# Performance work log

Measured on AMD Instinct MI355X. Metric: run time of the kernel, lower is better.

## Reference

```python
import jax, jax.numpy as jnp
import numpy as np

DIM = 1024

def setup_inputs() -> dict:
    key = jax.random.key(0)
    k1, k2, k3, k4 = jax.random.split(key, 4)
    B, L, D = 32, 2048, DIM
    x = jax.random.normal(k1, (B, D), dtype=jnp.float32)
    context = jax.random.normal(k2, (B, L, D), dtype=jnp.float32)
    # linear_concatWa: Linear(2*dim, dim, bias=False) -> weight [dim, 2*dim]
    Wa = jax.random.normal(k3, (D, 2 * D), dtype=jnp.float32) * (1.0 / np.sqrt(2 * D))
    # linear_concatVa: Linear(dim, 1, bias=False) -> weight [1, dim]
    Va = jax.random.normal(k4, (1, D), dtype=jnp.float32) * (1.0 / np.sqrt(D))
    return {"x": x, "context": context, "Wa": Wa, "Va": Va}


def reference(x, context, Wa, Va):
    # concat-mode additive (Bahdanau) attention.
    # Wa @ cat(ht, hs) == ht @ Wa[:, :D].T + hs @ Wa[:, D:].T  (avoids materializing concat)
    D = x.shape[-1]
    Wa_t, Wa_s = Wa[:, :D], Wa[:, D:]              # each [D, D]
    ht_proj = jnp.einsum('bd,kd->bk', x, Wa_t)     # [B, D]
    hs_proj = jnp.einsum('bld,kd->blk', context, Wa_s)  # [B, L, D]
    hidden = jnp.tanh(ht_proj[:, None, :] + hs_proj)    # [B, L, D]
    scores = jnp.einsum('blk,ok->bl', hidden, Va)       # [B, L]  (Va: [1, D])
    attn = jax.nn.softmax(scores, axis=-1)               # [B, L]
    weighted = jnp.einsum('bl,bld->bd', attn, context)   # [B, D]
    return weighted, attn
```

## Files before the change

### kernel.cpp

```cpp
#include <hip/hip_runtime.h>
#include <hip/hip_bf16.h>
#include <cstdint>
#include <cstddef>

#define DIM 1024
#define B_SZ 32
#define L_SZ 2048

#define BM 128
#define BN 128

#define CVT_BLOCKS 8192
#define HT_BLOCKS  512
#define WA_BLOCKS  512

typedef __attribute__((ext_vector_type(8))) short bf16x8;
typedef __attribute__((ext_vector_type(4))) float floatx4;

static __device__ __forceinline__ unsigned cvt2_bf16_rne(float a, float b) {
    unsigned ua = __builtin_bit_cast(unsigned, a);
    unsigned ub = __builtin_bit_cast(unsigned, b);
    ua = (ua + 0x7FFFu + ((ua >> 16) & 1u)) >> 16;
    ub = (ub + 0x7FFFu + ((ub >> 16) & 1u)) >> 16;
    return ua | (ub << 16);
}

static __device__ __forceinline__ float bf2f(unsigned u16) {
    return __builtin_bit_cast(float, u16 << 16);
}

static __device__ __forceinline__ float tanh_fast(float x) {
    float e = __expf(2.0f * x);
    return 1.0f - 2.0f * __builtin_amdgcn_rcpf(e + 1.0f);
}

static __device__ __forceinline__ void gld_lds16(const void* g, void* lds) {
    __builtin_amdgcn_global_load_lds(
        (const __attribute__((address_space(1))) unsigned int*)g,
        (__attribute__((address_space(3))) unsigned int*)lds,
        16, 0, 0);
}

__global__ __launch_bounds__(256) void pre_kernel(
    const float* __restrict__ x, const float* __restrict__ ctx,
    const float* __restrict__ Wa,
    unsigned short* __restrict__ ctxB, unsigned short* __restrict__ WaB,
    float* __restrict__ ht, float* __restrict__ scores,
    float* __restrict__ weighted)
{
    const int bid = blockIdx.x, t = threadIdx.x;

    if (bid < CVT_BLOCKS) {
        const long n4 = (long)B_SZ * L_SZ * DIM / 4;
        const long stride = (long)CVT_BLOCKS * 256;
        for (long i = (long)bid * 256 + t; i < n4; i += stride) {
            const float4 a = ((const float4*)ctx)[i];
            ((uint2*)ctxB)[i] =
                make_uint2(cvt2_bf16_rne(a.x, a.y), cvt2_bf16_rne(a.z, a.w));
        }
    } else if (bid < CVT_BLOCKS + HT_BLOCKS) {
        const int lb = bid - CVT_BLOCKS;
        const int gi = lb * 256 + t;
        if (gi < B_SZ * L_SZ) scores[gi] = 0.f;
        const int b = lb >> 4, kb = lb & 15;
        __shared__ float xs[DIM];
        for (int i = t; i < DIM; i += 256) xs[i] = x[b * DIM + i];
        __syncthreads();
        const int wave = t >> 6, lane = t & 63;
        const float4* xs4 = (const float4*)xs;
        for (int kk = 0; kk < 16; ++kk) {
            const int k = kb * 64 + wave * 16 + kk;
            const float4* wr = (const float4*)(Wa + (size_t)k * (2 * DIM));
            float s = 0.f;
            #pragma unroll
            for (int d = 0; d < DIM / 4; d += 64) {
                const float4 w4 = wr[d + lane];
                const float4 x4 = xs4[d + lane];
                s += w4.x * x4.x + w4.y * x4.y + w4.z * x4.z + w4.w * x4.w;
            }
            #pragma unroll
            for (int off = 32; off > 0; off >>= 1) s += __shfl_xor(s, off);
            if (lane == 0) ht[b * DIM + k] = s;
        }
    } else {
        const int lb = bid - CVT_BLOCKS - HT_BLOCKS;
        const int i = lb * 256 + t;
        if (i < B_SZ * DIM) weighted[i] = 0.f;
        const int k = i >> 7, dc = i & 127;
        const float* s = Wa + (size_t)k * (2 * DIM) + DIM + dc * 8;
        const float4 a = ((const float4*)s)[0];
        const float4 b4 = ((const float4*)s)[1];
        uint4 o;
        o.x = cvt2_bf16_rne(a.x, a.y);
        o.y = cvt2_bf16_rne(a.z, a.w);
        o.z = cvt2_bf16_rne(b4.x, b4.y);
        o.w = cvt2_bf16_rne(b4.z, b4.w);
        ((uint4*)(WaB + (size_t)k * DIM + dc * 8))[0] = o;
    }
}

__global__ __launch_bounds__(256) void gemm_score_bf16(
    const unsigned short* __restrict__ A, const unsigned short* __restrict__ Bm,
    const float* __restrict__ Va, const float* __restrict__ ht,
    float* __restrict__ scores)
{
    __shared__ __align__(16) unsigned short As[BM * 64];
    __shared__ __align__(16) unsigned short Bs[BN * 64];
    const int t = threadIdx.x;
    const int n0 = blockIdx.x * BN;
    const int m0 = blockIdx.y * BM;
    const int lane = t & 63, wave = t >> 6;
    const int l15 = lane & 15, quad = lane >> 4;
    const int wm = (wave >> 1) * 64, wn = (wave & 1) * 64;

    const int lr = lane >> 3;
    const int lc = (lane & 7) ^ lr;
    const size_t aRow = (size_t)(m0 + wave * 32 + lr);
    const size_t bRow = (size_t)(n0 + wave * 32 + lr);

    floatx4 acc[4][4];
    #pragma unroll
    for (int i = 0; i < 4; ++i)
        #pragma unroll
        for (int j = 0; j < 4; ++j) acc[i][j] = (floatx4)0.f;

    for (int k0 = 0; k0 < DIM; k0 += 64) {
        #pragma unroll
        for (int q = 0; q < 4; ++q) {
            gld_lds16(A + (aRow + q * 8) * DIM + k0 + lc * 8,
                      &As[(wave * 32 + q * 8) * 64]);
            gld_lds16(Bm + (bRow + q * 8) * DIM + k0 + lc * 8,
                      &Bs[(wave * 32 + q * 8) * 64]);
        }
        __syncthreads();

        bf16x8 af[2][4], bv[2][4];
        #pragma unroll
        for (int kb = 0; kb < 2; ++kb) {
            #pragma unroll
            for (int i = 0; i < 4; ++i) {
                const int r = wm + i * 16 + l15;
                const int c = (kb * 4 + quad) ^ (r & 7);
                af[kb][i] = *(const bf16x8*)&As[r * 64 + c * 8];
            }
            #pragma unroll
            for (int j = 0; j < 4; ++j) {
                const int r = wn + j * 16 + l15;
                const int c = (kb * 4 + quad) ^ (r & 7);
                bv[kb][j] = *(const bf16x8*)&Bs[r * 64 + c * 8];
            }
        }
        #pragma unroll
        for (int kb = 0; kb < 2; ++kb)
            #pragma unroll
            for (int i = 0; i < 4; ++i)
                #pragma unroll
                for (int j = 0; j < 4; ++j)
                    acc[i][j] = __builtin_amdgcn_mfma_f32_16x16x32_bf16(
                        af[kb][i], bv[kb][j], acc[i][j], 0, 0, 0);
        __syncthreads();
    }

    const int bb = m0 >> 11;
    float htv[4], vav[4];
    #pragma unroll
    for (int j = 0; j < 4; ++j) {
        const int ng = n0 + wn + j * 16 + l15;
        htv[j] = ht[bb * DIM + ng];
        vav[j] = Va[ng];
    }
    #pragma unroll
    for (int i = 0; i < 4; ++i) {
        #pragma unroll
        for (int r = 0; r < 4; ++r) {
            float s = 0.f;
            #pragma unroll
            for (int j = 0; j < 4; ++j)
                s += tanh_fast(acc[i][j][r] + htv[j]) * vav[j];
            s += __shfl_xor(s, 8);
            s += __shfl_xor(s, 4);
            s += __shfl_xor(s, 2);
            s += __shfl_xor(s, 1);
            if (l15 == 0)
                atomicAdd(&scores[m0 + wm + i * 16 + quad * 4 + r], s);
        }
    }
}

__global__ __launch_bounds__(256) void post_kernel(
    const float* __restrict__ scores, const unsigned short* __restrict__ ctxB,
    float* __restrict__ attn, float* __restrict__ weighted)
{
    const int b = blockIdx.x, slice = blockIdx.y, t = threadIdx.x;
    const float* sc = scores + b * L_SZ;
    __shared__ float red[256];
    __shared__ float att[128];

    float m = -1e30f;
    for (int l = t; l < L_SZ; l += 256) m = fmaxf(m, sc[l]);
    red[t] = m; __syncthreads();
    for (int s = 128; s > 0; s >>= 1) { if (t < s) red[t] = fmaxf(red[t], red[t + s]); __syncthreads(); }
    m = red[0]; __syncthreads();
    float sum = 0.f;
    for (int l = t; l < L_SZ; l += 256) sum += __expf(sc[l] - m);
    red[t] = sum; __syncthreads();
    for (int s = 128; s > 0; s >>= 1) { if (t < s) red[t] += red[t + s]; __syncthreads(); }
    const float inv = 1.0f / red[0];

    const int l0 = slice * 128;
    if (t < 128) {
        const float av = __expf(sc[l0 + t] - m) * inv;
        att[t] = av;
        attn[b * L_SZ + l0 + t] = av;
    }
    __syncthreads();

    const unsigned short* cb = ctxB + ((size_t)b * L_SZ + l0) * DIM + t * 4;
    float a0 = 0.f, a1 = 0.f, a2 = 0.f, a3 = 0.f;
    for (int l = 0; l < 128; ++l) {
        const float a = att[l];
        const uint2 v = *(const uint2*)(cb + (size_t)l * DIM);
        a0 += a * bf2f(v.x & 0xFFFFu);
        a1 += a * bf2f(v.x >> 16);
        a2 += a * bf2f(v.y & 0xFFFFu);
        a3 += a * bf2f(v.y >> 16);
    }
    float* o = weighted + b * DIM + t * 4;
    atomicAdd(o + 0, a0);
    atomicAdd(o + 1, a1);
    atomicAdd(o + 2, a2);
    atomicAdd(o + 3, a3);
}

#define LDS_STRIDE 40
__global__ __launch_bounds__(256) void ht_kernel_fb(const float* __restrict__ x,
                                                    const float* __restrict__ Wa,
                                                    float* __restrict__ ht,
                                                    float* __restrict__ scores) {
    const int b = blockIdx.x, kb = blockIdx.y, t = threadIdx.x;
    const int gidx = (b * 16 + kb) * 256 + t;
    if (gidx < B_SZ * L_SZ) scores[gidx] = 0.f;
    __shared__ float xs[DIM];
    for (int i = t; i < DIM; i += 256) xs[i] = x[b * DIM + i];
    __syncthreads();
    const int wave = t >> 6, lane = t & 63;
    for (int kk = 0; kk < 16; ++kk) {
        const int k = kb * 64 + wave * 16 + kk;
        const float* wr = Wa + (size_t)k * (2 * DIM);
        float s = 0.f;
        #pragma unroll
        for (int d = 0; d < DIM; d += 64) s += xs[d + lane] * wr[d + lane];
        #pragma unroll
        for (int off = 32; off > 0; off >>= 1) s += __shfl_xor(s, off);
        if (lane == 0) ht[b * DIM + k] = s;
    }
}

__global__ __launch_bounds__(256, 2) void gemm_score_kernel(
    const float* __restrict__ ctx, const float* __restrict__ Wa,
    const float* __restrict__ Va, const float* __restrict__ ht,
    float* __restrict__ scores)
{
    __shared__ unsigned short As[BM * LDS_STRIDE];
    __shared__ unsigned short Bs[BN * LDS_STRIDE];
    const int t = threadIdx.x;
    const int n0 = blockIdx.x * BN;
    const int m0 = blockIdx.y * BM;
    const int lane = t & 63, wave = t >> 6;
    const int l15 = lane & 15, quad = lane >> 4;
    const int wm = (wave >> 1) * 64, wn = (wave & 1) * 64;
    const int srow = t >> 3;
    const int scol = (t & 7) * 4;
    const float* aBase = ctx + (size_t)(m0 + srow) * DIM + scol;
    const float* bBase = Wa + (size_t)(n0 + srow) * (2 * DIM) + DIM + scol;

    floatx4 acc[4][4];
    #pragma unroll
    for (int i = 0; i < 4; ++i)
        #pragma unroll
        for (int j = 0; j < 4; ++j) acc[i][j] = (floatx4)0.f;

    for (int k0 = 0; k0 < DIM; k0 += 32) {
        __syncthreads();
        #pragma unroll
        for (int r = 0; r < 4; ++r) {
            const float4 va = *(const float4*)(aBase + (size_t)(r * 32) * DIM + k0);
            const float4 vb = *(const float4*)(bBase + (size_t)(r * 32) * (2 * DIM) + k0);
            *(uint2*)&As[(srow + r * 32) * LDS_STRIDE + scol] =
                make_uint2(cvt2_bf16_rne(va.x, va.y), cvt2_bf16_rne(va.z, va.w));
            *(uint2*)&Bs[(srow + r * 32) * LDS_STRIDE + scol] =
                make_uint2(cvt2_bf16_rne(vb.x, vb.y), cvt2_bf16_rne(vb.z, vb.w));
        }
        __syncthreads();
        bf16x8 af[4], bfr[4];
        #pragma unroll
        for (int i = 0; i < 4; ++i)
            af[i] = *(const bf16x8*)&As[(wm + i * 16 + l15) * LDS_STRIDE + quad * 8];
        #pragma unroll
        for (int j = 0; j < 4; ++j)
            bfr[j] = *(const bf16x8*)&Bs[(wn + j * 16 + l15) * LDS_STRIDE + quad * 8];
        #pragma unroll
        for (int i = 0; i < 4; ++i)
            #pragma unroll
            for (int j = 0; j < 4; ++j)
                acc[i][j] = __builtin_amdgcn_mfma_f32_16x16x32_bf16(af[i], bfr[j], acc[i][j], 0, 0, 0);
    }
    const int bb = m0 >> 11;
    float htv[4], vav[4];
    #pragma unroll
    for (int j = 0; j < 4; ++j) {
        const int ng = n0 + wn + j * 16 + l15;
        htv[j] = ht[bb * DIM + ng];
        vav[j] = Va[ng];
    }
    #pragma unroll
    for (int i = 0; i < 4; ++i) {
        #pragma unroll
        for (int r = 0; r < 4; ++r) {
            float s = 0.f;
            #pragma unroll
            for (int j = 0; j < 4; ++j)
                s += tanh_fast(acc[i][j][r] + htv[j]) * vav[j];
            s += __shfl_xor(s, 8);
            s += __shfl_xor(s, 4);
            s += __shfl_xor(s, 2);
            s += __shfl_xor(s, 1);
            if (l15 == 0)
                atomicAdd(&scores[m0 + wm + i * 16 + quad * 4 + r], s);
        }
    }
}

__global__ __launch_bounds__(256) void post_kernel_fb(
    const float* __restrict__ scores, const float* __restrict__ ctx,
    float* __restrict__ attn, float* __restrict__ weighted)
{
    const int b = blockIdx.x, slice = blockIdx.y, t = threadIdx.x;
    const float* sc = scores + b * L_SZ;
    __shared__ float red[256];
    __shared__ float att[128];
    float m = -1e30f;
    for (int l = t; l < L_SZ; l += 256) m = fmaxf(m, sc[l]);
    red[t] = m; __syncthreads();
    for (int s = 128; s > 0; s >>= 1) { if (t < s) red[t] = fmaxf(red[t], red[t + s]); __syncthreads(); }
    m = red[0]; __syncthreads();
    float sum = 0.f;
    for (int l = t; l < L_SZ; l += 256) sum += __expf(sc[l] - m);
    red[t] = sum; __syncthreads();
    for (int s = 128; s > 0; s >>= 1) { if (t < s) red[t] += red[t + s]; __syncthreads(); }
    const float inv = 1.0f / red[0];
    const int l0 = slice * 128;
    if (t < 128) {
        const float av = __expf(sc[l0 + t] - m) * inv;
        att[t] = av;
        attn[b * L_SZ + l0 + t] = av;
    }
    __syncthreads();
    const float* cb = ctx + ((size_t)b * L_SZ + l0) * DIM + t * 4;
    float4 w = make_float4(0.f, 0.f, 0.f, 0.f);
    for (int l = 0; l < 128; ++l) {
        const float a = att[l];
        const float4 c = *(const float4*)(cb + (size_t)l * DIM);
        w.x += a * c.x; w.y += a * c.y; w.z += a * c.z; w.w += a * c.w;
    }
    float* o = weighted + b * DIM + t * 4;
    atomicAdd(o + 0, w.x);
    atomicAdd(o + 1, w.y);
    atomicAdd(o + 2, w.z);
    atomicAdd(o + 3, w.w);
}

__global__ __launch_bounds__(256) void zero_weighted_fb(float* __restrict__ weighted) {
    const int i = blockIdx.x * 256 + threadIdx.x;
    if (i < B_SZ * DIM) weighted[i] = 0.f;
}

extern "C" void kernel_launch(void* const* d_in, const int* in_sizes, int n_in,
                              void* d_out, int out_size, void* d_ws, size_t ws_size,
                              hipStream_t stream) {
    const float* x   = (const float*)d_in[0];
    const float* ctx = (const float*)d_in[1];
    const float* Wa  = (const float*)d_in[2];
    const float* Va  = (const float*)d_in[3];

    float* out      = (float*)d_out;
    float* weighted = out;
    float* attn     = out + B_SZ * DIM;

    float* scores = (float*)d_ws;
    float* ht     = scores + B_SZ * L_SZ;

    const size_t base = (size_t)(B_SZ * L_SZ + B_SZ * DIM) * sizeof(float);
    const size_t need = base + (size_t)DIM * DIM * 2
                      + (size_t)B_SZ * L_SZ * DIM * 2;

    if (ws_size >= need) {
        unsigned short* WaB  = (unsigned short*)((char*)d_ws + base);
        unsigned short* ctxB = WaB + (size_t)DIM * DIM;
        pre_kernel<<<CVT_BLOCKS + HT_BLOCKS + WA_BLOCKS, 256, 0, stream>>>(
            x, ctx, Wa, ctxB, WaB, ht, scores, weighted);
        gemm_score_bf16<<<dim3(DIM / BN, (B_SZ * L_SZ) / BM), 256, 0, stream>>>(
            ctxB, WaB, Va, ht, scores);
        post_kernel<<<dim3(B_SZ, 16), 256, 0, stream>>>(scores, ctxB, attn, weighted);
    } else {
        ht_kernel_fb<<<dim3(B_SZ, 16), 256, 0, stream>>>(x, Wa, ht, scores);
        zero_weighted_fb<<<(B_SZ * DIM + 255) / 256, 256, 0, stream>>>(weighted);
        gemm_score_kernel<<<dim3(DIM / BN, (B_SZ * L_SZ) / BM), 256, 0, stream>>>(
            ctx, Wa, Va, ht, scores);
        post_kernel_fb<<<dim3(B_SZ, 16), 256, 0, stream>>>(scores, ctx, attn, weighted);
    }
}
```

Measured before the change: 603.3 us.

## Fuse context bf16 conversion into GEMM A-tile load, drop bf16 copy

Removes the separate pass that converts the whole fp32 context tensor to a bf16 workspace copy. The GEMM now loads fp32 context, rounds it to bf16 in registers and writes it into the swizzled LDS tile, and the post kernel reads fp32 context directly. This is meant to cut the large write-then-reread of a bf16 context copy. In exchange, the GEMM fetches twice as many bytes per A tile, repeated across column blocks, and uses register staging instead of direct-to-LDS loads. Rounding changes from round-to-nearest-even to round-half-up.

```diff
diff --git a/kernel.cpp b/kernel.cpp
--- a/kernel.cpp
+++ b/kernel.cpp
@@ -10,7 +10,6 @@
 #define BM 128
 #define BN 128
 
-#define CVT_BLOCKS 8192
 #define HT_BLOCKS  512
 #define WA_BLOCKS  512
 
@@ -25,8 +24,10 @@
     return ua | (ub << 16);
 }
 
-static __device__ __forceinline__ float bf2f(unsigned u16) {
-    return __builtin_bit_cast(float, u16 << 16);
+static __device__ __forceinline__ unsigned pk2_bf16_rhu(float a, float b) {
+    const unsigned ua = __builtin_bit_cast(unsigned, a) + 0x8000u;
+    const unsigned ub = __builtin_bit_cast(unsigned, b) + 0x8000u;
+    return __builtin_amdgcn_perm(ub, ua, 0x07060302u);
 }
 
 static __device__ __forceinline__ float tanh_fast(float x) {
@@ -42,24 +43,15 @@
 }
 
 __global__ __launch_bounds__(256) void pre_kernel(
-    const float* __restrict__ x, const float* __restrict__ ctx,
-    const float* __restrict__ Wa,
-    unsigned short* __restrict__ ctxB, unsigned short* __restrict__ WaB,
+    const float* __restrict__ x, const float* __restrict__ Wa,
+    unsigned short* __restrict__ WaB,
     float* __restrict__ ht, float* __restrict__ scores,
     float* __restrict__ weighted)
 {
     const int bid = blockIdx.x, t = threadIdx.x;
 
-    if (bid < CVT_BLOCKS) {
-        const long n4 = (long)B_SZ * L_SZ * DIM / 4;
-        const long stride = (long)CVT_BLOCKS * 256;
-        for (long i = (long)bid * 256 + t; i < n4; i += stride) {
-            const float4 a = ((const float4*)ctx)[i];
-            ((uint2*)ctxB)[i] =
-                make_uint2(cvt2_bf16_rne(a.x, a.y), cvt2_bf16_rne(a.z, a.w));
-        }
-    } else if (bid < CVT_BLOCKS + HT_BLOCKS) {
-        const int lb = bid - CVT_BLOCKS;
+    if (bid < HT_BLOCKS) {
+        const int lb = bid;
         const int gi = lb * 256 + t;
         if (gi < B_SZ * L_SZ) scores[gi] = 0.f;
         const int b = lb >> 4, kb = lb & 15;
@@ -83,7 +75,7 @@
             if (lane == 0) ht[b * DIM + k] = s;
         }
     } else {
-        const int lb = bid - CVT_BLOCKS - HT_BLOCKS;
+        const int lb = bid - HT_BLOCKS;
         const int i = lb * 256 + t;
         if (i < B_SZ * DIM) weighted[i] = 0.f;
         const int k = i >> 7, dc = i & 127;
@@ -99,8 +91,8 @@
     }
 }
 
-__global__ __launch_bounds__(256) void gemm_score_bf16(
-    const unsigned short* __restrict__ A, const unsigned short* __restrict__ Bm,
+__global__ __launch_bounds__(256) void gemm_score_f32a(
+    const float* __restrict__ A, const unsigned short* __restrict__ Bm,
     const float* __restrict__ Va, const float* __restrict__ ht,
     float* __restrict__ scores)
 {
@@ -113,10 +105,14 @@
     const int l15 = lane & 15, quad = lane >> 4;
     const int wm = (wave >> 1) * 64, wn = (wave & 1) * 64;
 
-    const int lr = lane >> 3;
-    const int lc = (lane & 7) ^ lr;
-    const size_t aRow = (size_t)(m0 + wave * 32 + lr);
-    const size_t bRow = (size_t)(n0 + wave * 32 + lr);
+    const int lrB = lane >> 3;
+    const int lcB = (lane & 7) ^ lrB;
+    const size_t bRow = (size_t)(n0 + wave * 32 + lrB);
+
+    const int lrA = lane >> 4;
+    const int ccA = lane & 15;
+    const size_t aRowBase = (size_t)(m0 + wave * 32 + lrA);
+    const int hA = ccA & 1;
 
     floatx4 acc[4][4];
     #pragma unroll
@@ -126,11 +122,17 @@
 
     for (int k0 = 0; k0 < DIM; k0 += 64) {
         #pragma unroll
-        for (int q = 0; q < 4; ++q) {
-            gld_lds16(A + (aRow + q * 8) * DIM + k0 + lc * 8,
-                      &As[(wave * 32 + q * 8) * 64]);
-            gld_lds16(Bm + (bRow + q * 8) * DIM + k0 + lc * 8,
+        for (int q = 0; q < 4; ++q)
+            gld_lds16(Bm + (bRow + q * 8) * DIM + k0 + lcB * 8,
                       &Bs[(wave * 32 + q * 8) * 64]);
+
+        #pragma unroll
+        for (int q = 0; q < 8; ++q) {
+            const int r = wave * 32 + q * 4 + lrA;
+            const float4 v = *(const float4*)(A + (aRowBase + q * 4) * DIM + k0 + ccA * 4);
+            const uint2 p = make_uint2(pk2_bf16_rhu(v.x, v.y), pk2_bf16_rhu(v.z, v.w));
+            const int c = ((ccA >> 1) ^ (r & 7));
+            *(uint2*)&As[r * 64 + c * 8 + hA * 4] = p;
         }
         __syncthreads();
 
@@ -188,7 +190,7 @@
 }
 
 __global__ __launch_bounds__(256) void post_kernel(
-    const float* __restrict__ scores, const unsigned short* __restrict__ ctxB,
+    const float* __restrict__ scores, const float* __restrict__ ctx,
     float* __restrict__ attn, float* __restrict__ weighted)
 {
     const int b = blockIdx.x, slice = blockIdx.y, t = threadIdx.x;
@@ -215,31 +217,30 @@
     }
     __syncthreads();
 
-    const unsigned short* cb = ctxB + ((size_t)b * L_SZ + l0) * DIM + t * 4;
-    float a0 = 0.f, a1 = 0.f, a2 = 0.f, a3 = 0.f;
+    const float* cb = ctx + ((size_t)b * L_SZ + l0) * DIM + t * 4;
+    float4 w = make_float4(0.f, 0.f, 0.f, 0.f);
     for (int l = 0; l < 128; ++l) {
         const float a = att[l];
-        const uint2 v = *(const uint2*)(cb + (size_t)l * DIM);
-        a0 += a * bf2f(v.x & 0xFFFFu);
-        a1 += a * bf2f(v.x >> 16);
-        a2 += a * bf2f(v.y & 0xFFFFu);
-        a3 += a * bf2f(v.y >> 16);
+        const float4 c = *(const float4*)(cb + (size_t)l * DIM);
+        w.x += a * c.x; w.y += a * c.y; w.z += a * c.z; w.w += a * c.w;
     }
     float* o = weighted + b * DIM + t * 4;
-    atomicAdd(o + 0, a0);
-    atomicAdd(o + 1, a1);
-    atomicAdd(o + 2, a2);
-    atomicAdd(o + 3, a3);
+    atomicAdd(o + 0, w.x);
+    atomicAdd(o + 1, w.y);
+    atomicAdd(o + 2, w.z);
+    atomicAdd(o + 3, w.w);
 }
 
 #define LDS_STRIDE 40
 __global__ __launch_bounds__(256) void ht_kernel_fb(const float* __restrict__ x,
                                                     const float* __restrict__ Wa,
                                                     float* __restrict__ ht,
-                                                    float* __restrict__ scores) {
+                                                    float* __restrict__ scores,
+                                                    float* __restrict__ weighted) {
     const int b = blockIdx.x, kb = blockIdx.y, t = threadIdx.x;
     const int gidx = (b * 16 + kb) * 256 + t;
     if (gidx < B_SZ * L_SZ) scores[gidx] = 0.f;
+    if (gidx < B_SZ * DIM) weighted[gidx] = 0.f;
     __shared__ float xs[DIM];
     for (int i = t; i < DIM; i += 256) xs[i] = x[b * DIM + i];
     __syncthreads();
@@ -331,50 +332,6 @@
     }
 }
 
-__global__ __launch_bounds__(256) void post_kernel_fb(
-    const float* __restrict__ scores, const float* __restrict__ ctx,
-    float* __restrict__ attn, float* __restrict__ weighted)
-{
-    const int b = blockIdx.x, slice = blockIdx.y, t = threadIdx.x;
-    const float* sc = scores + b * L_SZ;
-    __shared__ float red[256];
-    __shared__ float att[128];
-    float m = -1e30f;
-    for (int l = t; l < L_SZ; l += 256) m = fmaxf(m, sc[l]);
-    red[t] = m; __syncthreads();
-    for (int s = 128; s > 0; s >>= 1) { if (t < s) red[t] = fmaxf(red[t], red[t + s]); __syncthreads(); }
-    m = red[0]; __syncthreads();
-    float sum = 0.f;
-    for (int l = t; l < L_SZ; l += 256) sum += __expf(sc[l] - m);
-    red[t] = sum; __syncthreads();
-    for (int s = 128; s > 0; s >>= 1) { if (t < s) red[t] += red[t + s]; __syncthreads(); }
-    const float inv = 1.0f / red[0];
-    const int l0 = slice * 128;
-    if (t < 128) {
-        const float av = __expf(sc[l0 + t] - m) * inv;
-        att[t] = av;
-        attn[b * L_SZ + l0 + t] = av;
-    }
-    __syncthreads();
-    const float* cb = ctx + ((size_t)b * L_SZ + l0) * DIM + t * 4;
-    float4 w = make_float4(0.f, 0.f, 0.f, 0.f);
-    for (int l = 0; l < 128; ++l) {
-        const float a = att[l];
-        const float4 c = *(const float4*)(cb + (size_t)l * DIM);
-        w.x += a * c.x; w.y += a * c.y; w.z += a * c.z; w.w += a * c.w;
-    }
-    float* o = weighted + b * DIM + t * 4;
-    atomicAdd(o + 0, w.x);
-    atomicAdd(o + 1, w.y);
-    atomicAdd(o + 2, w.z);
-    atomicAdd(o + 3, w.w);
-}
-
-__global__ __launch_bounds__(256) void zero_weighted_fb(float* __restrict__ weighted) {
-    const int i = blockIdx.x * 256 + threadIdx.x;
-    if (i < B_SZ * DIM) weighted[i] = 0.f;
-}
-
 extern "C" void kernel_launch(void* const* d_in, const int* in_sizes, int n_in,
                               void* d_out, int out_size, void* d_ws, size_t ws_size,
                               hipStream_t stream) {
@@ -391,22 +348,19 @@
     float* ht     = scores + B_SZ * L_SZ;
 
     const size_t base = (size_t)(B_SZ * L_SZ + B_SZ * DIM) * sizeof(float);
-    const size_t need = base + (size_t)DIM * DIM * 2
-                      + (size_t)B_SZ * L_SZ * DIM * 2;
+    const size_t need = base + (size_t)DIM * DIM * 2;
 
     if (ws_size >= need) {
-        unsigned short* WaB  = (unsigned short*)((char*)d_ws + base);
-        unsigned short* ctxB = WaB + (size_t)DIM * DIM;
-        pre_kernel<<<CVT_BLOCKS + HT_BLOCKS + WA_BLOCKS, 256, 0, stream>>>(
-            x, ctx, Wa, ctxB, WaB, ht, scores, weighted);
-        gemm_score_bf16<<<dim3(DIM / BN, (B_SZ * L_SZ) / BM), 256, 0, stream>>>(
-            ctxB, WaB, Va, ht, scores);
-        post_kernel<<<dim3(B_SZ, 16), 256, 0, stream>>>(scores, ctxB, attn, weighted);
+        unsigned short* WaB = (unsigned short*)((char*)d_ws + base);
+        pre_kernel<<<HT_BLOCKS + WA_BLOCKS, 256, 0, stream>>>(
+            x, Wa, WaB, ht, scores, weighted);
+        gemm_score_f32a<<<dim3(DIM / BN, (B_SZ * L_SZ) / BM), 256, 0, stream>>>(
+            ctx, WaB, Va, ht, scores);
+        post_kernel<<<dim3(B_SZ, 16), 256, 0, stream>>>(scores, ctx, attn, weighted);
     } else {
-        ht_kernel_fb<<<dim3(B_SZ, 16), 256, 0, stream>>>(x, Wa, ht, scores);
-        zero_weighted_fb<<<(B_SZ * DIM + 255) / 256, 256, 0, stream>>>(weighted);
+        ht_kernel_fb<<<dim3(B_SZ, 16), 256, 0, stream>>>(x, Wa, ht, scores, weighted);
         gemm_score_kernel<<<dim3(DIM / BN, (B_SZ * L_SZ) / BM), 256, 0, stream>>>(
             ctx, Wa, Va, ht, scores);
-        post_kernel_fb<<<dim3(B_SZ, 16), 256, 0, stream>>>(scores, ctx, attn, weighted);
-    }
-}
+        post_kernel<<<dim3(B_SZ, 16), 256, 0, stream>>>(scores, ctx, attn, weighted);
+    }
+}
```

New measurement: 648.4 us. 7.5% more time.
